# Kernel optimization log

Measured on AMD Instinct MI355X. Metric: run time of the kernel, lower is better.

The kernel has to match this reference:

```python
import jax, jax.numpy as jnp
import numpy as np

EPS = 1e-5
SLOPE = 0.01  # torch LeakyReLU default


def _leaky(x):
    return jnp.where(x > 0, x, SLOPE * x)


def _layernorm(x, g, b):
    mu = jnp.mean(x, axis=-1, keepdims=True)
    var = jnp.var(x, axis=-1, keepdims=True)
    return (x - mu) * jax.lax.rsqrt(var + EPS) * g + b


def setup_inputs() -> dict:
    key = jax.random.key(0)
    B, N, E, L = 1, 512, 256, 64
    D = E + L  # 320
    ks = jax.random.split(key, 16)
    p = {}
    p["robot_embedding"] = jax.random.normal(ks[0], (B, N, E), jnp.float32)
    p["object_embedding"] = jax.random.normal(ks[1], (B, N, E), jnp.float32)
    p["language_emb"] = jax.random.normal(ks[2], (B, L), jnp.float32)
    # MLPKernel params: Linear(2D->D) + LN + LeakyReLU, Linear(D->D) + LN + LeakyReLU, Linear(D->1)
    p["W1"] = jax.random.normal(ks[3], (2 * D, D), jnp.float32) * 0.02
    p["b1"] = jnp.zeros((D,), jnp.float32)
    p["g1"] = jnp.ones((D,), jnp.float32)
    p["be1"] = jnp.zeros((D,), jnp.float32)
    p["W2"] = jax.random.normal(ks[4], (D, D), jnp.float32) * 0.02
    p["b2"] = jnp.zeros((D,), jnp.float32)
    p["g2"] = jnp.ones((D,), jnp.float32)
    p["be2"] = jnp.zeros((D,), jnp.float32)
    p["W3"] = jax.random.normal(ks[5], (D, 1), jnp.float32) * 0.02
    p["b3"] = jnp.zeros((1,), jnp.float32)
    return p


def _forward(robot_embedding, object_embedding, language_emb,
             W1, b1, g1, be1, W2, b2, g2, be2, W3, b3):
    B, N, E = robot_embedding.shape
    # use_language=True path: z = language_emb, broadcast over N and concat
    z = jnp.broadcast_to(language_emb[:, None, :], (B, N, language_emb.shape[-1]))
    Phi_A = jnp.concatenate([robot_embedding, z], axis=-1)   # [B,N,D]
    Phi_B = jnp.concatenate([object_embedding, z], axis=-1)  # [B,N,D]
    D = Phi_A.shape[-1]
    # Pairwise concat [B,N,N,2D] == kernel(Phi_A_r, Phi_B_r) on the full grid.
    # Equivalent to the block_computing loop (same math, different tiling).
    fA = jnp.broadcast_to(Phi_A[:, :, None, :], (B, N, N, D))
    fB = jnp.broadcast_to(Phi_B[:, None, :, :], (B, N, N, D))
    feat = jnp.concatenate([fA, fB], axis=-1)  # [B,N,N,2D]
    h = _leaky(_layernorm(feat @ W1 + b1, g1, be1))
    h = _leaky(_layernorm(h @ W2 + b2, g2, be2))
    dro = jnp.abs((h @ W3 + b3)[..., 0])  # [B,N,N]
    return dro


def reference(robot_embedding, object_embedding, language_emb,
              W1, b1, g1, be1, W2, b2, g2, be2, W3, b3):
    dro = _forward(robot_embedding, object_embedding, language_emb,
                   W1, b1, g1, be1, W2, b2, g2, be2, W3, b3)
    # outputs = {'dro': dro, 'mu': None, 'logvar': None} -> return dro
    return dro
```

## Files before the change

kernel.cpp:

```cpp
#include <hip/hip_runtime.h>
#include <hip/hip_bf16.h>

#define LN_EPS 1e-5f
#define SLOPE 0.01f

typedef short bf16x8 __attribute__((ext_vector_type(8)));
typedef float f32x4 __attribute__((ext_vector_type(4)));

__global__ __launch_bounds__(320) void precompute_uv(
    const float* __restrict__ robot, const float* __restrict__ object,
    const float* __restrict__ lang, const float* __restrict__ W1,
    const float* __restrict__ b1, float* __restrict__ U, float* __restrict__ V,
    __hip_bfloat16* __restrict__ Ub, __hip_bfloat16* __restrict__ Vb,
    float* __restrict__ stats)
{
  __shared__ float red[5][2];
  const int i = blockIdx.x;
  const int d = threadIdx.x;
  const int isV = blockIdx.y;
  const float* __restrict__ src   = isV ? object : robot;
  const float* __restrict__ Wbase = W1 + (isV ? 320 * 320 : 0);

  float acc = 0.f;
#pragma unroll 8
  for (int k = 0; k < 256; ++k)
    acc = fmaf(src[i * 256 + k], Wbase[k * 320 + d], acc);
#pragma unroll 8
  for (int l = 0; l < 64; ++l)
    acc = fmaf(lang[l], Wbase[(256 + l) * 320 + d], acc);
  if (isV) acc += b1[d];

  (isV ? V : U)[i * 320 + d] = acc;
  (isV ? Vb : Ub)[i * 320 + d] = __float2bfloat16(acc);

  float s = acc, q = acc * acc;
#pragma unroll
  for (int m = 1; m < 64; m <<= 1) {
    s += __shfl_xor(s, m);
    q += __shfl_xor(q, m);
  }
  const int w = d >> 6, lane = d & 63;
  if (lane == 0) { red[w][0] = s; red[w][1] = q; }
  __syncthreads();
  if (d == 0) {
    float s0 = 0.f, q0 = 0.f;
    for (int t = 0; t < 5; ++t) { s0 += red[t][0]; q0 += red[t][1]; }
    stats[isV * 1024 + i] = s0;
    stats[isV * 1024 + 512 + i] = q0;
  }
}

__global__ __launch_bounds__(256) void dot_and_reorder(
    const __hip_bfloat16* __restrict__ Ub, const __hip_bfloat16* __restrict__ Vb,
    float* __restrict__ DOT, const float* __restrict__ W2,
    __hip_bfloat16* __restrict__ W2F)
{
  if (blockIdx.x < 256) {
    const int w = threadIdx.x >> 6, lane = threadIdx.x & 63;
    const int id = blockIdx.x * 4 + w;
    const int ti = id >> 5, tj = id & 31;
    const int r16 = lane & 15, g = lane >> 4;
    f32x4 acc = (f32x4){0.f, 0.f, 0.f, 0.f};
    const __hip_bfloat16* __restrict__ A = Ub + (ti * 16 + r16) * 320;
    const __hip_bfloat16* __restrict__ B = Vb + (tj * 16 + r16) * 320;
#pragma unroll
    for (int kk = 0; kk < 10; ++kk) {
      bf16x8 a = *(const bf16x8*)(A + kk * 32 + g * 8);
      bf16x8 b = *(const bf16x8*)(B + kk * 32 + g * 8);
      acc = __builtin_amdgcn_mfma_f32_16x16x32_bf16(a, b, acc, 0, 0, 0);
    }
#pragma unroll
    for (int r = 0; r < 4; ++r)
      DOT[(ti * 16 + g * 4 + r) * 512 + tj * 16 + r16] = acc[r];
  } else {
    __shared__ float tile[32][33];
    const int t = blockIdx.x - 256;
    const int d0 = (t % 10) * 32;
    const int kk = t / 10;
    const int tx = threadIdx.x & 31, ty = threadIdx.x >> 5;
#pragma unroll
    for (int r = 0; r < 32; r += 8)
      tile[ty + r][tx] = W2[((kk * 32) + ty + r) * 320 + d0 + tx];
    __syncthreads();
    const int fl   = threadIdx.x >> 7;
    const int l    = (threadIdx.x >> 1) & 63;
    const int half = threadIdx.x & 1;
    const int frag = (d0 >> 4) + fl;
    __hip_bfloat16* dst = W2F + ((kk * 20 + frag) * 512) + l * 8 + half * 4;
#pragma unroll
    for (int e = 0; e < 4; ++e)
      dst[e] = __float2bfloat16(tile[(l >> 4) * 8 + half * 4 + e]
                                    [fl * 16 + (l & 15)]);
  }
}

__global__ __launch_bounds__(256, 3) void fused_main(
    const float* __restrict__ U, const float* __restrict__ V,
    const __hip_bfloat16* __restrict__ W2F,
    const float* __restrict__ DOT, const float* __restrict__ stats,
    const float* __restrict__ g1, const float* __restrict__ be1,
    const float* __restrict__ b2, const float* __restrict__ g2,
    const float* __restrict__ be2, const float* __restrict__ W3,
    const float* __restrict__ b3, float* __restrict__ out)
{
  __shared__ __align__(16) __hip_bfloat16 h1[64 * 320];
  __shared__ __align__(16) float U_lds[320], g1_lds[320], be1_lds[320];
  __shared__ float mu_lds[64], rs_lds[64];
  __shared__ float part[64][4][2];
  __shared__ float pdot[64][4];

  const int i   = blockIdx.x;
  const int j0  = blockIdx.y * 64;
  const int tid = threadIdx.x;
  const int lane = tid & 63;
  const int w    = tid >> 6;
  const int r16  = lane & 15;
  const int g    = lane >> 4;

  for (int t = tid; t < 320; t += 256) {
    U_lds[t]   = U[i * 320 + t];
    g1_lds[t]  = g1[t];
    be1_lds[t] = be1[t];
  }
  if (tid >= 192) {
    const int r = tid - 192;
    const float sU = stats[i],             qU = stats[512 + i];
    const float sV = stats[1024 + j0 + r], qV = stats[1536 + j0 + r];
    const float dt = DOT[i * 512 + j0 + r];
    const float mu = (sU + sV) * (1.f / 320.f);
    const float var = (qU + 2.f * dt + qV) * (1.f / 320.f) - mu * mu;
    mu_lds[r] = mu;
    rs_lds[r] = rsqrtf(var + LN_EPS);
  }
  __syncthreads();

  {
    const int row = tid >> 2, seg = tid & 3;
    const float* __restrict__ Vrow = V + (j0 + row) * 320 + seg * 80;
    const float rs = rs_lds[row];
    const float murs = mu_lds[row] * rs;
    const unsigned swz = (unsigned)((row & 7) << 4);
    const unsigned base = (unsigned)row * 640u + (unsigned)seg * 160u;
#pragma unroll
    for (int m = 0; m < 10; ++m) {
      const int d = seg * 80 + m * 8;
      const f32x4 va = *(const f32x4*)(Vrow + m * 8);
      const f32x4 vb = *(const f32x4*)(Vrow + m * 8 + 4);
      const f32x4 ua = *(const f32x4*)&U_lds[d];
      const f32x4 ub = *(const f32x4*)&U_lds[d + 4];
      const f32x4 ga = *(const f32x4*)&g1_lds[d];
      const f32x4 gb = *(const f32x4*)&g1_lds[d + 4];
      const f32x4 ea = *(const f32x4*)&be1_lds[d];
      const f32x4 eb = *(const f32x4*)&be1_lds[d + 4];
      union { bf16x8 v; __hip_bfloat16 e[8]; } pk;
#pragma unroll
      for (int e = 0; e < 4; ++e) {
        const float x = ua[e] + va[e];
        float hv = fmaf(fmaf(x, rs, -murs), ga[e], ea[e]);
        hv = fmaxf(hv, SLOPE * hv);
        pk.e[e] = __float2bfloat16(hv);
      }
#pragma unroll
      for (int e = 0; e < 4; ++e) {
        const float x = ub[e] + vb[e];
        float hv = fmaf(fmaf(x, rs, -murs), gb[e], eb[e]);
        hv = fmaxf(hv, SLOPE * hv);
        pk.e[4 + e] = __float2bfloat16(hv);
      }
      *(bf16x8*)((char*)h1 + ((base + (unsigned)m * 16u) ^ swz)) = pk.v;
    }
  }
  __syncthreads();

  const int wc = w;
  f32x4 acc[4][5];
#pragma unroll
  for (int mf = 0; mf < 4; ++mf)
#pragma unroll
    for (int nf = 0; nf < 5; ++nf)
      acc[mf][nf] = (f32x4){0.f, 0.f, 0.f, 0.f};

  const __hip_bfloat16* __restrict__ Bf = W2F + (size_t)(wc * 5) * 512 + lane * 8;
  const unsigned swzA = (unsigned)((r16 & 7) << 4);
  unsigned arow[4];
#pragma unroll
  for (int mf = 0; mf < 4; ++mf)
    arow[mf] = (unsigned)(mf * 16 + r16) * 640u;

  bf16x8 bbuf[2][5];
#pragma unroll
  for (int nf = 0; nf < 5; ++nf)
    bbuf[0][nf] = *(const bf16x8*)(Bf + nf * 512);

#pragma unroll
  for (int kk = 0; kk < 10; ++kk) {
    const int cur = kk & 1, nxt = cur ^ 1;
    if (kk < 9) {
#pragma unroll
      for (int nf = 0; nf < 5; ++nf)
        bbuf[nxt][nf] = *(const bf16x8*)(Bf + ((kk + 1) * 20 + nf) * 512);
    }
    const unsigned k2 = (unsigned)((kk * 32 + g * 8) * 2);
    bf16x8 a[4];
#pragma unroll
    for (int mf = 0; mf < 4; ++mf)
      a[mf] = *(const bf16x8*)((const char*)h1 + ((arow[mf] + k2) ^ swzA));
#pragma unroll
    for (int nf = 0; nf < 5; ++nf)
#pragma unroll
      for (int mf = 0; mf < 4; ++mf)
        acc[mf][nf] = __builtin_amdgcn_mfma_f32_16x16x32_bf16(
            a[mf], bbuf[cur][nf], acc[mf][nf], 0, 0, 0);
  }

  float b2c[5], g2c[5], be2c[5], w3c[5];
#pragma unroll
  for (int nf = 0; nf < 5; ++nf) {
    const int col = wc * 80 + nf * 16 + r16;
    b2c[nf]  = b2[col];
    g2c[nf]  = g2[col];
    be2c[nf] = be2[col];
    w3c[nf]  = W3[col];
  }
#pragma unroll
  for (int nf = 0; nf < 5; ++nf)
#pragma unroll
    for (int mf = 0; mf < 4; ++mf)
#pragma unroll
      for (int r = 0; r < 4; ++r)
        acc[mf][nf][r] += b2c[nf];

#pragma unroll
  for (int mf = 0; mf < 4; ++mf) {
#pragma unroll
    for (int r = 0; r < 4; ++r) {
      float s = 0.f, q = 0.f;
#pragma unroll
      for (int nf = 0; nf < 5; ++nf) {
        const float v = acc[mf][nf][r];
        s += v;
        q = fmaf(v, v, q);
      }
#pragma unroll
      for (int m = 1; m < 16; m <<= 1) {
        s += __shfl_xor(s, m);
        q += __shfl_xor(q, m);
      }
      if (r16 == 0) {
        const int row = mf * 16 + g * 4 + r;
        part[row][wc][0] = s;
        part[row][wc][1] = q;
      }
    }
  }
  __syncthreads();

#pragma unroll
  for (int mf = 0; mf < 4; ++mf) {
#pragma unroll
    for (int r = 0; r < 4; ++r) {
      const int row = mf * 16 + g * 4 + r;
      const float s = part[row][0][0] + part[row][1][0] +
                      part[row][2][0] + part[row][3][0];
      const float q = part[row][0][1] + part[row][1][1] +
                      part[row][2][1] + part[row][3][1];
      const float mu  = s * (1.f / 320.f);
      const float var = q * (1.f / 320.f) - mu * mu;
      const float rs  = rsqrtf(var + LN_EPS);
      const float murs = mu * rs;
      float dsum = 0.f;
#pragma unroll
      for (int nf = 0; nf < 5; ++nf) {
        float v = fmaf(fmaf(acc[mf][nf][r], rs, -murs), g2c[nf], be2c[nf]);
        v = fmaxf(v, SLOPE * v);
        dsum = fmaf(v, w3c[nf], dsum);
      }
#pragma unroll
      for (int m = 1; m < 16; m <<= 1)
        dsum += __shfl_xor(dsum, m);
      if (r16 == 0)
        pdot[row][wc] = dsum;
    }
  }
  __syncthreads();

  if (tid < 64) {
    const float tot = pdot[tid][0] + pdot[tid][1] + pdot[tid][2] +
                      pdot[tid][3] + b3[0];
    out[i * 512 + j0 + tid] = fabsf(tot);
  }
}

extern "C" void kernel_launch(void* const* d_in, const int* in_sizes, int n_in,
                              void* d_out, int out_size, void* d_ws, size_t ws_size,
                              hipStream_t stream) {
  const float* robot  = (const float*)d_in[0];
  const float* object = (const float*)d_in[1];
  const float* lang   = (const float*)d_in[2];
  const float* W1  = (const float*)d_in[3];
  const float* b1  = (const float*)d_in[4];
  const float* g1  = (const float*)d_in[5];
  const float* be1 = (const float*)d_in[6];
  const float* W2  = (const float*)d_in[7];
  const float* b2  = (const float*)d_in[8];
  const float* g2  = (const float*)d_in[9];
  const float* be2 = (const float*)d_in[10];
  const float* W3  = (const float*)d_in[11];
  const float* b3  = (const float*)d_in[12];
  float* out = (float*)d_out;

  float* U     = (float*)d_ws;
  float* V     = U + 512 * 320;
  float* stats = V + 512 * 320;
  float* DOT   = stats + 2048;
  __hip_bfloat16* W2F = (__hip_bfloat16*)(DOT + 512 * 512);
  __hip_bfloat16* Ub  = W2F + 320 * 320;
  __hip_bfloat16* Vb  = Ub + 512 * 320;

  precompute_uv<<<dim3(512, 2), 320, 0, stream>>>(robot, object, lang, W1, b1,
                                                  U, V, Ub, Vb, stats);
  dot_and_reorder<<<356, 256, 0, stream>>>(Ub, Vb, DOT, W2, W2F);
  fused_main<<<dim3(512, 8), 256, 0, stream>>>(U, V, W2F, DOT, stats,
                                               g1, be1, b2, g2, be2, W3, b3,
                                               out);
}
```

Baseline: 215.0 us.

## Compute U·V dot inline in main kernel and merge prep kernels

Drops the separate MFMA kernel that built the U·V dot-product matrix. The main kernel now loads each V row into registers, computes the dot product with U in fp32 using a 4-lane shuffle reduction, and reuses those registers for the layer-1 LayerNorm. The W2 reorder work moves into the U/V precompute kernel, which cuts three launches to two and removes the DOT, Ub and Vb workspace traffic. In exchange the main kernel carries 80 extra registers of V data, which could lower occupancy, and it repeats the dot-product work for every block.

```diff
diff --git a/kernel.cpp b/kernel.cpp
--- a/kernel.cpp
+++ b/kernel.cpp
@@ -7,97 +7,79 @@
 typedef short bf16x8 __attribute__((ext_vector_type(8)));
 typedef float f32x4 __attribute__((ext_vector_type(4)));
 
-__global__ __launch_bounds__(320) void precompute_uv(
+__global__ __launch_bounds__(320) void prep_kernel(
     const float* __restrict__ robot, const float* __restrict__ object,
     const float* __restrict__ lang, const float* __restrict__ W1,
-    const float* __restrict__ b1, float* __restrict__ U, float* __restrict__ V,
-    __hip_bfloat16* __restrict__ Ub, __hip_bfloat16* __restrict__ Vb,
-    float* __restrict__ stats)
+    const float* __restrict__ b1, const float* __restrict__ W2,
+    float* __restrict__ U, float* __restrict__ V,
+    float* __restrict__ stats, __hip_bfloat16* __restrict__ W2F)
 {
   __shared__ float red[5][2];
-  const int i = blockIdx.x;
-  const int d = threadIdx.x;
-  const int isV = blockIdx.y;
-  const float* __restrict__ src   = isV ? object : robot;
-  const float* __restrict__ Wbase = W1 + (isV ? 320 * 320 : 0);
-
-  float acc = 0.f;
+  __shared__ float tile[32][33];
+  const int bx = blockIdx.x;
+  const int tid = threadIdx.x;
+
+  if (bx < 1024) {
+    const int i = bx >> 1;
+    const int isV = bx & 1;
+    const int d = tid;
+    const float* __restrict__ src   = isV ? object : robot;
+    const float* __restrict__ Wbase = W1 + (isV ? 320 * 320 : 0);
+
+    float acc = 0.f;
 #pragma unroll 8
-  for (int k = 0; k < 256; ++k)
-    acc = fmaf(src[i * 256 + k], Wbase[k * 320 + d], acc);
+    for (int k = 0; k < 256; ++k)
+      acc = fmaf(src[i * 256 + k], Wbase[k * 320 + d], acc);
 #pragma unroll 8
-  for (int l = 0; l < 64; ++l)
-    acc = fmaf(lang[l], Wbase[(256 + l) * 320 + d], acc);
-  if (isV) acc += b1[d];
-
-  (isV ? V : U)[i * 320 + d] = acc;
-  (isV ? Vb : Ub)[i * 320 + d] = __float2bfloat16(acc);
-
-  float s = acc, q = acc * acc;
-#pragma unroll
-  for (int m = 1; m < 64; m <<= 1) {
-    s += __shfl_xor(s, m);
-    q += __shfl_xor(q, m);
-  }
-  const int w = d >> 6, lane = d & 63;
-  if (lane == 0) { red[w][0] = s; red[w][1] = q; }
-  __syncthreads();
-  if (d == 0) {
-    float s0 = 0.f, q0 = 0.f;
-    for (int t = 0; t < 5; ++t) { s0 += red[t][0]; q0 += red[t][1]; }
-    stats[isV * 1024 + i] = s0;
-    stats[isV * 1024 + 512 + i] = q0;
-  }
-}
-
-__global__ __launch_bounds__(256) void dot_and_reorder(
-    const __hip_bfloat16* __restrict__ Ub, const __hip_bfloat16* __restrict__ Vb,
-    float* __restrict__ DOT, const float* __restrict__ W2,
-    __hip_bfloat16* __restrict__ W2F)
-{
-  if (blockIdx.x < 256) {
-    const int w = threadIdx.x >> 6, lane = threadIdx.x & 63;
-    const int id = blockIdx.x * 4 + w;
-    const int ti = id >> 5, tj = id & 31;
-    const int r16 = lane & 15, g = lane >> 4;
-    f32x4 acc = (f32x4){0.f, 0.f, 0.f, 0.f};
-    const __hip_bfloat16* __restrict__ A = Ub + (ti * 16 + r16) * 320;
-    const __hip_bfloat16* __restrict__ B = Vb + (tj * 16 + r16) * 320;
-#pragma unroll
-    for (int kk = 0; kk < 10; ++kk) {
-      bf16x8 a = *(const bf16x8*)(A + kk * 32 + g * 8);
-      bf16x8 b = *(const bf16x8*)(B + kk * 32 + g * 8);
-      acc = __builtin_amdgcn_mfma_f32_16x16x32_bf16(a, b, acc, 0, 0, 0);
-    }
-#pragma unroll
-    for (int r = 0; r < 4; ++r)
-      DOT[(ti * 16 + g * 4 + r) * 512 + tj * 16 + r16] = acc[r];
+    for (int l = 0; l < 64; ++l)
+      acc = fmaf(lang[l], Wbase[(256 + l) * 320 + d], acc);
+    if (isV) acc += b1[d];
+
+    (isV ? V : U)[i * 320 + d] = acc;
+
+    float s = acc, q = acc * acc;
+#pragma unroll
+    for (int m = 1; m < 64; m <<= 1) {
+      s += __shfl_xor(s, m);
+      q += __shfl_xor(q, m);
+    }
+    const int w = d >> 6, lane = d & 63;
+    if (lane == 0) { red[w][0] = s; red[w][1] = q; }
+    __syncthreads();
+    if (d == 0) {
+      float s0 = 0.f, q0 = 0.f;
+      for (int t = 0; t < 5; ++t) { s0 += red[t][0]; q0 += red[t][1]; }
+      stats[isV * 1024 + i] = s0;
+      stats[isV * 1024 + 512 + i] = q0;
+    }
   } else {
-    __shared__ float tile[32][33];
-    const int t = blockIdx.x - 256;
+    const int t = bx - 1024;
     const int d0 = (t % 10) * 32;
     const int kk = t / 10;
-    const int tx = threadIdx.x & 31, ty = threadIdx.x >> 5;
-#pragma unroll
-    for (int r = 0; r < 32; r += 8)
-      tile[ty + r][tx] = W2[((kk * 32) + ty + r) * 320 + d0 + tx];
+    if (tid < 256) {
+      const int tx = tid & 31, ty = tid >> 5;
+#pragma unroll
+      for (int r = 0; r < 32; r += 8)
+        tile[ty + r][tx] = W2[((kk * 32) + ty + r) * 320 + d0 + tx];
+    }
     __syncthreads();
-    const int fl   = threadIdx.x >> 7;
-    const int l    = (threadIdx.x >> 1) & 63;
-    const int half = threadIdx.x & 1;
-    const int frag = (d0 >> 4) + fl;
-    __hip_bfloat16* dst = W2F + ((kk * 20 + frag) * 512) + l * 8 + half * 4;
-#pragma unroll
-    for (int e = 0; e < 4; ++e)
-      dst[e] = __float2bfloat16(tile[(l >> 4) * 8 + half * 4 + e]
-                                    [fl * 16 + (l & 15)]);
+    if (tid < 256) {
+      const int fl   = tid >> 7;
+      const int l    = (tid >> 1) & 63;
+      const int half = tid & 1;
+      const int frag = (d0 >> 4) + fl;
+      __hip_bfloat16* dst = W2F + ((kk * 20 + frag) * 512) + l * 8 + half * 4;
+#pragma unroll
+      for (int e = 0; e < 4; ++e)
+        dst[e] = __float2bfloat16(tile[(l >> 4) * 8 + half * 4 + e]
+                                      [fl * 16 + (l & 15)]);
+    }
   }
 }
 
 __global__ __launch_bounds__(256, 3) void fused_main(
     const float* __restrict__ U, const float* __restrict__ V,
-    const __hip_bfloat16* __restrict__ W2F,
-    const float* __restrict__ DOT, const float* __restrict__ stats,
+    const __hip_bfloat16* __restrict__ W2F, const float* __restrict__ stats,
     const float* __restrict__ g1, const float* __restrict__ be1,
     const float* __restrict__ b2, const float* __restrict__ g2,
     const float* __restrict__ be2, const float* __restrict__ W3,
@@ -105,7 +87,6 @@
 {
   __shared__ __align__(16) __hip_bfloat16 h1[64 * 320];
   __shared__ __align__(16) float U_lds[320], g1_lds[320], be1_lds[320];
-  __shared__ float mu_lds[64], rs_lds[64];
   __shared__ float part[64][4][2];
   __shared__ float pdot[64][4];
 
@@ -116,36 +97,55 @@
   const int w    = tid >> 6;
   const int r16  = lane & 15;
   const int g    = lane >> 4;
+  const int row  = tid >> 2;
+  const int seg  = tid & 3;
+
+  const float* __restrict__ Vrow = V + (j0 + row) * 320 + seg * 80;
+  f32x4 vreg[20];
+#pragma unroll
+  for (int m = 0; m < 20; ++m)
+    vreg[m] = *(const f32x4*)(Vrow + m * 4);
+  const float sVr = stats[1024 + j0 + row];
+  const float qVr = stats[1536 + j0 + row];
+
+  const int wc = w;
+  const __hip_bfloat16* __restrict__ Bf = W2F + (size_t)(wc * 5) * 512 + lane * 8;
+  bf16x8 bbuf[2][5];
+#pragma unroll
+  for (int nf = 0; nf < 5; ++nf)
+    bbuf[0][nf] = *(const bf16x8*)(Bf + nf * 512);
 
   for (int t = tid; t < 320; t += 256) {
     U_lds[t]   = U[i * 320 + t];
     g1_lds[t]  = g1[t];
     be1_lds[t] = be1[t];
   }
-  if (tid >= 192) {
-    const int r = tid - 192;
-    const float sU = stats[i],             qU = stats[512 + i];
-    const float sV = stats[1024 + j0 + r], qV = stats[1536 + j0 + r];
-    const float dt = DOT[i * 512 + j0 + r];
-    const float mu = (sU + sV) * (1.f / 320.f);
-    const float var = (qU + 2.f * dt + qV) * (1.f / 320.f) - mu * mu;
-    mu_lds[r] = mu;
-    rs_lds[r] = rsqrtf(var + LN_EPS);
-  }
+  const float sU = stats[i], qU = stats[512 + i];
   __syncthreads();
 
+  float dt = 0.f;
+#pragma unroll
+  for (int m = 0; m < 20; ++m) {
+    const f32x4 u = *(const f32x4*)&U_lds[seg * 80 + m * 4];
+#pragma unroll
+    for (int e = 0; e < 4; ++e)
+      dt = fmaf(u[e], vreg[m][e], dt);
+  }
+  dt += __shfl_xor(dt, 1);
+  dt += __shfl_xor(dt, 2);
+  const float mu   = (sU + sVr) * (1.f / 320.f);
+  const float var  = (qU + 2.f * dt + qVr) * (1.f / 320.f) - mu * mu;
+  const float rs   = rsqrtf(var + LN_EPS);
+  const float murs = mu * rs;
+
   {
-    const int row = tid >> 2, seg = tid & 3;
-    const float* __restrict__ Vrow = V + (j0 + row) * 320 + seg * 80;
-    const float rs = rs_lds[row];
-    const float murs = mu_lds[row] * rs;
-    const unsigned swz = (unsigned)((row & 7) << 4);
+    const unsigned swz  = (unsigned)((row & 7) << 4);
     const unsigned base = (unsigned)row * 640u + (unsigned)seg * 160u;
 #pragma unroll
     for (int m = 0; m < 10; ++m) {
       const int d = seg * 80 + m * 8;
-      const f32x4 va = *(const f32x4*)(Vrow + m * 8);
-      const f32x4 vb = *(const f32x4*)(Vrow + m * 8 + 4);
+      const f32x4 va = vreg[2 * m];
+      const f32x4 vb = vreg[2 * m + 1];
       const f32x4 ua = *(const f32x4*)&U_lds[d];
       const f32x4 ub = *(const f32x4*)&U_lds[d + 4];
       const f32x4 ga = *(const f32x4*)&g1_lds[d];
@@ -172,7 +172,6 @@
   }
   __syncthreads();
 
-  const int wc = w;
   f32x4 acc[4][5];
 #pragma unroll
   for (int mf = 0; mf < 4; ++mf)
@@ -180,17 +179,11 @@
     for (int nf = 0; nf < 5; ++nf)
       acc[mf][nf] = (f32x4){0.f, 0.f, 0.f, 0.f};
 
-  const __hip_bfloat16* __restrict__ Bf = W2F + (size_t)(wc * 5) * 512 + lane * 8;
   const unsigned swzA = (unsigned)((r16 & 7) << 4);
   unsigned arow[4];
 #pragma unroll
   for (int mf = 0; mf < 4; ++mf)
     arow[mf] = (unsigned)(mf * 16 + r16) * 640u;
-
-  bf16x8 bbuf[2][5];
-#pragma unroll
-  for (int nf = 0; nf < 5; ++nf)
-    bbuf[0][nf] = *(const bf16x8*)(Bf + nf * 512);
 
 #pragma unroll
   for (int kk = 0; kk < 10; ++kk) {
@@ -247,9 +240,9 @@
         q += __shfl_xor(q, m);
       }
       if (r16 == 0) {
-        const int row = mf * 16 + g * 4 + r;
-        part[row][wc][0] = s;
-        part[row][wc][1] = q;
+        const int rw = mf * 16 + g * 4 + r;
+        part[rw][wc][0] = s;
+        part[rw][wc][1] = q;
       }
     }
   }
@@ -259,19 +252,19 @@
   for (int mf = 0; mf < 4; ++mf) {
 #pragma unroll
     for (int r = 0; r < 4; ++r) {
-      const int row = mf * 16 + g * 4 + r;
-      const float s = part[row][0][0] + part[row][1][0] +
-                      part[row][2][0] + part[row][3][0];
-      const float q = part[row][0][1] + part[row][1][1] +
-                      part[row][2][1] + part[row][3][1];
-      const float mu  = s * (1.f / 320.f);
-      const float var = q * (1.f / 320.f) - mu * mu;
-      const float rs  = rsqrtf(var + LN_EPS);
-      const float murs = mu * rs;
+      const int rw = mf * 16 + g * 4 + r;
+      const float s = part[rw][0][0] + part[rw][1][0] +
+                      part[rw][2][0] + part[rw][3][0];
+      const float q = part[rw][0][1] + part[rw][1][1] +
+                      part[rw][2][1] + part[rw][3][1];
+      const float mu2  = s * (1.f / 320.f);
+      const float var2 = q * (1.f / 320.f) - mu2 * mu2;
+      const float rs2  = rsqrtf(var2 + LN_EPS);
+      const float murs2 = mu2 * rs2;
       float dsum = 0.f;
 #pragma unroll
       for (int nf = 0; nf < 5; ++nf) {
-        float v = fmaf(fmaf(acc[mf][nf][r], rs, -murs), g2c[nf], be2c[nf]);
+        float v = fmaf(fmaf(acc[mf][nf][r], rs2, -murs2), g2c[nf], be2c[nf]);
         v = fmaxf(v, SLOPE * v);
         dsum = fmaf(v, w3c[nf], dsum);
       }
@@ -279,7 +272,7 @@
       for (int m = 1; m < 16; m <<= 1)
         dsum += __shfl_xor(dsum, m);
       if (r16 == 0)
-        pdot[row][wc] = dsum;
+        pdot[rw][wc] = dsum;
     }
   }
   __syncthreads();
@@ -312,15 +305,11 @@
   float* U     = (float*)d_ws;
   float* V     = U + 512 * 320;
   float* stats = V + 512 * 320;
-  float* DOT   = stats + 2048;
-  __hip_bfloat16* W2F = (__hip_bfloat16*)(DOT + 512 * 512);
-  __hip_bfloat16* Ub  = W2F + 320 * 320;
-  __hip_bfloat16* Vb  = Ub + 512 * 320;
-
-  precompute_uv<<<dim3(512, 2), 320, 0, stream>>>(robot, object, lang, W1, b1,
-                                                  U, V, Ub, Vb, stats);
-  dot_and_reorder<<<356, 256, 0, stream>>>(Ub, Vb, DOT, W2, W2F);
-  fused_main<<<dim3(512, 8), 256, 0, stream>>>(U, V, W2F, DOT, stats,
+  __hip_bfloat16* W2F = (__hip_bfloat16*)(stats + 2048);
+
+  prep_kernel<<<1124, 320, 0, stream>>>(robot, object, lang, W1, b1, W2,
+                                        U, V, stats, W2F);
+  fused_main<<<dim3(512, 8), 256, 0, stream>>>(U, V, W2F, stats,
                                                g1, be1, b2, g2, be2, W3, b3,
                                                out);
 }
```

New measurement: 213.4 us. Within noise of the previous version (-0.8%).
